# Performance work log

Measured on AMD Instinct MI355X. Metric: run time of the kernel, lower is better.

The kernel has to match this reference:

```python
import jax, jax.numpy as jnp
import numpy as np
from math import comb

B = 2048          # num_batch
NVAR = 11         # Bernstein coefficients per axis
NUM = 100         # trajectory time samples
NUM_OBS = 10
MAXITER = 50
T_FIN = 5.0
A_OBS = 0.4; B_OBS = 0.4
RHO_OBS = 1.0; RHO_INEQ = 1.0; RHO_TARGET = 1.0; RHO_PROJ = 1.0
V_MIN = 0.1; V_MAX = 2.0; A_MAX = 2.0


def _bernstein(n, t):
    return np.stack([comb(n, k) * t**k * (1.0 - t)**(n - k) for k in range(n + 1)], axis=1)


def _basis_matrices():
    # Bernstein polynomial basis of degree NVAR-1 sampled at NUM points over [0, T_FIN]
    t = np.linspace(0.0, 1.0, NUM)
    n = NVAR - 1
    P = _bernstein(n, t)
    Bm1 = _bernstein(n - 1, t)
    Bm2 = _bernstein(n - 2, t)
    dP = np.zeros_like(P); ddP = np.zeros_like(P)
    for k in range(n + 1):
        d = np.zeros(NUM)
        if k > 0: d += Bm1[:, k - 1]
        if k < n: d -= Bm1[:, k]
        dP[:, k] = n * d / T_FIN
        dd = np.zeros(NUM)
        if k > 1: dd += Bm2[:, k - 2]
        if 0 < k < n: dd -= 2.0 * Bm2[:, k - 1]
        if k < n - 1: dd += Bm2[:, k]
        ddP[:, k] = n * (n - 1) * dd / T_FIN**2
    return (jnp.asarray(P, jnp.float32), jnp.asarray(dP, jnp.float32), jnp.asarray(ddP, jnp.float32))


def setup_inputs() -> dict:
    key = jax.random.key(0)
    ks = jax.random.split(key, 10)
    P, Pdot, Pddot = _basis_matrices()
    u = lambda k, s, lo, hi: jax.random.uniform(k, s, jnp.float32, lo, hi)
    init_state_ego = jnp.concatenate([u(ks[0], (B, 2), -1.0, 1.0), u(ks[1], (B, 2), 0.1, 1.0)], axis=1)
    term_states = jnp.concatenate([u(ks[2], (B, 2), 2.0, 6.0), u(ks[3], (B, 2), 0.1, 1.0)], axis=1)
    via_points = u(ks[4], (B, 4), 0.5, 4.0)
    closest_obs = u(ks[5], (B, 2 * NUM_OBS), -4.0, 4.0)
    target_init = jnp.concatenate([u(ks[6], (B, 2), 1.0, 5.0), u(ks[7], (B, 2), -0.5, 0.5)], axis=1)
    d_min_t = u(ks[8], (B, 1), 1.0, 1.5)
    d_max_t = d_min_t + u(ks[9], (B, 1), 0.5, 1.0)
    d_target_bounds = jnp.concatenate([d_min_t, d_max_t], axis=1)
    return {"P": P, "Pdot": Pdot, "Pddot": Pddot, "init_state_ego": init_state_ego,
            "term_states": term_states, "via_points": via_points, "closest_obs": closest_obs,
            "target_init": target_init, "d_target_bounds": d_target_bounds}


def reference(P, Pdot, Pddot, init_state_ego, term_states, via_points, closest_obs, target_init, d_target_bounds):
    dt = P.dtype
    tot_time = jnp.linspace(0.0, T_FIN, NUM, dtype=dt)
    A_via = jnp.stack([P[49], P[74]])
    A_eq_init = jnp.vstack([P[0], Pdot[0], P[-1], Pdot[-1], A_via])   # [6, NVAR]
    A_eq = jnp.vstack([P[0], Pdot[0], P[-1], Pdot[-1]])               # [4, NVAR]
    A_obs_mat = jnp.tile(P, (NUM_OBS, 1))                             # [NUM_OBS*NUM, NVAR]
    A_vel, A_acc, A_target = Pdot, Pddot, P

    def kkt_inv(cost, A):
        m = A.shape[0]
        M = jnp.vstack([jnp.hstack([cost, A.T]), jnp.hstack([A, jnp.zeros((m, m), dt)])])
        return jnp.linalg.inv(M)

    inv_init = kkt_inv(Pddot.T @ Pddot, A_eq_init)
    cost_opt = (RHO_OBS * A_obs_mat.T @ A_obs_mat + RHO_INEQ * A_acc.T @ A_acc
                + RHO_INEQ * A_vel.T @ A_vel + RHO_TARGET * A_target.T @ A_target
                + RHO_PROJ * jnp.eye(NVAR, dtype=dt))
    inv_opt = kkt_inv(cost_opt, A_eq)

    zeros1 = jnp.zeros((B, 1), dt)
    vx0, vy0 = init_state_ego[:, 2:3], init_state_ego[:, 3:4]
    x_term, y_term = term_states[:, 0:1], term_states[:, 1:2]
    vx_term, vy_term = term_states[:, 2:3], term_states[:, 3:4]

    # warm-start QP (equality-constrained, zero linear cost): qp_layer_init
    b_eq_x_init = jnp.hstack([zeros1, vx0, x_term, vx_term, via_points[:, 0:2]])
    b_eq_y_init = jnp.hstack([zeros1, vy0, y_term, vy_term, via_points[:, 2:4]])
    zlin = jnp.zeros((B, NVAR), dt)
    c_x_bar = (jnp.hstack([zlin, b_eq_x_init]) @ inv_init.T)[:, :NVAR]
    c_y_bar = (jnp.hstack([zlin, b_eq_y_init]) @ inv_init.T)[:, :NVAR]

    b_eq_x = jnp.hstack([zeros1, vx0, x_term, vx_term])
    b_eq_y = jnp.hstack([zeros1, vy0, y_term, vy_term])

    # constant-velocity target trajectory, [B, NUM]
    x_target = target_init[:, 0:1] + target_init[:, 2:3] * tot_time[None, :]
    y_target = target_init[:, 1:2] + target_init[:, 3:4] * tot_time[None, :]

    # static obstacles tiled over time (obs-major, time fastest), [B, NUM_OBS*NUM]
    x_obs_traj = jnp.repeat(closest_obs[:, :NUM_OBS], NUM, axis=1)
    y_obs_traj = jnp.repeat(closest_obs[:, NUM_OBS:2 * NUM_OBS], NUM, axis=1)
    d_min_t, d_max_t = d_target_bounds[:, 0:1], d_target_bounds[:, 1:2]

    def step(carry, _):
        primal, lx, ly = carry
        cx, cy = primal[:, :NVAR], primal[:, NVAR:]
        x, xdot, xddot = cx @ P.T, cx @ Pdot.T, cx @ Pddot.T
        y, ydot, yddot = cy @ P.T, cy @ Pdot.T, cy @ Pddot.T
        # obstacle avoidance polar reformulation (compute_alph_d)
        wc = jnp.tile(x, (1, NUM_OBS)) - x_obs_traj
        ws = jnp.tile(y, (1, NUM_OBS)) - y_obs_traj
        a_o = jnp.arctan2(ws * A_OBS, wc * B_OBS)
        ca, sa = jnp.cos(a_o), jnp.sin(a_o)
        c1 = RHO_OBS * (A_OBS**2 * ca**2 + B_OBS**2 * sa**2)
        c2 = RHO_OBS * (A_OBS * wc * ca + B_OBS * ws * sa)
        d_obs = jnp.maximum(jnp.ones_like(c2), c2 / c1)
        # velocity bound (rho_ineq cancels in c2/c1)
        a_v = jnp.arctan2(ydot, xdot); cv, sv = jnp.cos(a_v), jnp.sin(a_v)
        d_v = jnp.clip(xdot * cv + ydot * sv, V_MIN, V_MAX)
        # acceleration bound
        a_a = jnp.arctan2(yddot, xddot); cA, sA = jnp.cos(a_a), jnp.sin(a_a)
        d_a = jnp.clip(xddot * cA + yddot * sA, 0.0, A_MAX)
        # target distance band
        wct, wst = x - x_target, y - y_target
        bt = jnp.arctan2(wst, wct); cb, sb = jnp.cos(bt), jnp.sin(bt)
        d_t = jnp.clip(wct * cb + wst * sb, d_min_t, d_max_t)
        # residuals -> dual (lambda) update
        res_xo = wc - A_OBS * d_obs * ca; res_yo = ws - B_OBS * d_obs * sa
        res_vx = xdot - d_v * cv;         res_vy = ydot - d_v * sv
        res_ax = xddot - d_a * cA;        res_ay = yddot - d_a * sA
        res_tx = wct - d_t * cb;          res_ty = wst - d_t * sb
        lx = lx - RHO_OBS * res_xo @ A_obs_mat - RHO_INEQ * res_ax @ A_acc - RHO_INEQ * res_vx @ A_vel - RHO_TARGET * res_tx @ A_target
        ly = ly - RHO_OBS * res_yo @ A_obs_mat - RHO_INEQ * res_ay @ A_acc - RHO_INEQ * res_vy @ A_vel - RHO_TARGET * res_ty @ A_target
        # linear cost and closed-form KKT solve (A_projection = I)
        b_ox = x_obs_traj + A_OBS * d_obs * ca; b_oy = y_obs_traj + B_OBS * d_obs * sa
        b_tx = x_target + d_t * cb;             b_ty = y_target + d_t * sb
        lin_x = (-lx - RHO_OBS * b_ox @ A_obs_mat - RHO_INEQ * (d_a * cA) @ A_acc
                 - RHO_INEQ * (d_v * cv) @ A_vel - RHO_TARGET * b_tx @ A_target - RHO_PROJ * c_x_bar)
        lin_y = (-ly - RHO_OBS * b_oy @ A_obs_mat - RHO_INEQ * (d_a * sA) @ A_acc
                 - RHO_INEQ * (d_v * sv) @ A_vel - RHO_TARGET * b_ty @ A_target - RHO_PROJ * c_y_bar)
        new_cx = (jnp.hstack([-lin_x, b_eq_x]) @ inv_opt.T)[:, :NVAR]
        new_cy = (jnp.hstack([-lin_y, b_eq_y]) @ inv_opt.T)[:, :NVAR]
        return (jnp.hstack([new_cx, new_cy]), lx, ly), None

    init = (jnp.hstack([c_x_bar, c_y_bar]), jnp.zeros((B, NVAR), dt), jnp.zeros((B, NVAR), dt))
    (primal, lx, ly), _ = jax.lax.scan(jax.checkpoint(step), init, None, length=MAXITER)
    return primal
```

## Files before the change

kernel.cpp:

```cpp
#include <hip/hip_runtime.h>
#include <math.h>

#define NVARS 11
#define NUMT  100
#define NOBS  10
#define MAXIT 50

#define E_OFF    0
#define F_OFF    66
#define G4_OFF   187
#define GP_OFF   231
#define GPD_OFF  352
#define GPDD_OFF 473
#define WS_FLOATS 594

__device__ void gj_inv(double (*aug)[34], int N, double* fac, int* piv, int tid, int nthr)
{
    for (int k = 0; k < N; ++k) {
        if (tid == 0) {
            int p = k; double best = fabs(aug[k][k]);
            for (int r = k + 1; r < N; ++r) { double v = fabs(aug[r][k]); if (v > best) { best = v; p = r; } }
            *piv = p;
        }
        __syncthreads();
        int p = *piv;
        if (p != k) {
            for (int c = tid; c < 2 * N; c += nthr) { double t = aug[k][c]; aug[k][c] = aug[p][c]; aug[p][c] = t; }
        }
        __syncthreads();
        double pv = aug[k][k];
        __syncthreads();
        for (int c = tid; c < 2 * N; c += nthr) aug[k][c] /= pv;
        __syncthreads();
        if (tid < N) fac[tid] = aug[tid][k];
        __syncthreads();
        for (int idx = tid; idx < N * 2 * N; idx += nthr) {
            int r = idx / (2 * N), c = idx % (2 * N);
            if (r != k) aug[r][c] -= fac[r] * aug[k][c];
        }
        __syncthreads();
    }
}

__global__ __launch_bounds__(128) void setup_kernel(const float* __restrict__ P,
                                                    const float* __restrict__ Pd,
                                                    const float* __restrict__ Pdd,
                                                    float* __restrict__ ws)
{
    __shared__ double G[3][NVARS][NVARS];
    __shared__ double aug[17][34];
    __shared__ double fac[17];
    __shared__ int piv;
    const int tid = threadIdx.x, nthr = 128;

    for (int idx = tid; idx < 3 * 121; idx += nthr) {
        int q = idx / 121, rem = idx % 121, r = rem / 11, c = rem % 11;
        const float* B = (q == 0) ? P : (q == 1) ? Pd : Pdd;
        double s = 0.0;
        for (int t = 0; t < NUMT; ++t) s += (double)B[t * 11 + r] * (double)B[t * 11 + c];
        G[q][r][c] = s;
    }
    __syncthreads();
    for (int idx = tid; idx < 3 * 121; idx += nthr) ws[GP_OFF + idx] = (float)((&G[0][0][0])[idx]);

    for (int idx = tid; idx < 17 * 34; idx += nthr) aug[idx / 34][idx % 34] = 0.0;
    __syncthreads();
    for (int idx = tid; idx < 121; idx += nthr) aug[idx / 11][idx % 11] = G[2][idx / 11][idx % 11];
    if (tid < 66) {
        int r = tid / 11, j = tid % 11;
        const float* src = (r == 0) ? P : (r == 1) ? Pd : (r == 2) ? (P + 99 * 11) : (r == 3) ? (Pd + 99 * 11)
                           : (r == 4) ? (P + 49 * 11) : (P + 74 * 11);
        double v = (double)src[j];
        aug[j][11 + r] = v;
        aug[11 + r][j] = v;
    }
    if (tid < 17) aug[tid][17 + tid] = 1.0;
    __syncthreads();
    gj_inv(aug, 17, fac, &piv, tid, nthr);
    if (tid < 66) { int j = tid / 6, k = tid % 6; ws[E_OFF + tid] = (float)aug[j][17 + 11 + k]; }
    __syncthreads();

    for (int idx = tid; idx < 17 * 34; idx += nthr) aug[idx / 34][idx % 34] = 0.0;
    __syncthreads();
    for (int idx = tid; idx < 121; idx += nthr) {
        int r = idx / 11, c = idx % 11;
        aug[r][c] = 11.0 * G[0][r][c] + G[1][r][c] + G[2][r][c] + ((r == c) ? 1.0 : 0.0);
    }
    if (tid < 44) {
        int r = tid / 11, j = tid % 11;
        const float* src = (r == 0) ? P : (r == 1) ? Pd : (r == 2) ? (P + 99 * 11) : (Pd + 99 * 11);
        double v = (double)src[j];
        aug[j][11 + r] = v;
        aug[11 + r][j] = v;
    }
    if (tid < 15) aug[tid][15 + tid] = 1.0;
    __syncthreads();
    gj_inv(aug, 15, fac, &piv, tid, nthr);
    if (tid < 121) { int j = tid / 11, k = tid % 11; ws[F_OFF + tid] = (float)aug[j][15 + k]; }
    if (tid < 44)  { int j = tid / 4,  k = tid % 4;  ws[G4_OFF + tid] = (float)aug[j][15 + 11 + k]; }
}

__device__ __forceinline__ float sbcast(float v) {
    return __int_as_float(__builtin_amdgcn_readfirstlane(__float_as_int(v)));
}

__global__ __launch_bounds__(256, 4) void solve_kernel(
    const float* __restrict__ P, const float* __restrict__ Pd, const float* __restrict__ Pdd,
    const float* __restrict__ ise, const float* __restrict__ term, const float* __restrict__ via,
    const float* __restrict__ obs, const float* __restrict__ tgt, const float* __restrict__ dtb,
    const float* __restrict__ ws, float* __restrict__ out, int Btot)
{
    __shared__ __align__(16) float sBc[NVARS][304];
    __shared__ __align__(16) float wbc[2][2][304];
    __shared__ float cst[WS_FLOATS];
    __shared__ float Dred[2][6][12];
    __shared__ float mlin[2][2][12];
    __shared__ float scoef[2][2][12];
    __shared__ float beqs[2][2][4];
    __shared__ float sobs[2][2][NOBS];
    __shared__ float stgt[2][6];

    const int tid = threadIdx.x;
    const int l = tid & 127;
    const int e = tid >> 7;
    int b = blockIdx.x * 2 + e;
    const bool real = (b < Btot);
    if (!real) b = Btot - 1;

    for (int idx = tid; idx < NVARS * 304; idx += 256) {
        int j = idx / 304, r = idx % 304;
        float v = 0.f;
        if (r < 300) {
            int q = r / 100, t = r % 100;
            const float* Bq = (q == 0) ? P : (q == 1) ? Pd : Pdd;
            v = Bq[t * 11 + j];
        }
        sBc[j][r] = v;
    }
    for (int idx = tid; idx < WS_FLOATS; idx += 256) cst[idx] = ws[idx];
    if (l < 20) sobs[e][l / 10][l % 10] = obs[b * 20 + l];
    if (l == 0) {
        beqs[e][0][0] = 0.f; beqs[e][0][1] = ise[b*4+2]; beqs[e][0][2] = term[b*4+0]; beqs[e][0][3] = term[b*4+2];
        beqs[e][1][0] = 0.f; beqs[e][1][1] = ise[b*4+3]; beqs[e][1][2] = term[b*4+1]; beqs[e][1][3] = term[b*4+3];
        stgt[e][0] = tgt[b*4+0]; stgt[e][1] = tgt[b*4+2];
        stgt[e][2] = tgt[b*4+1]; stgt[e][3] = tgt[b*4+3];
        stgt[e][4] = dtb[b*2+0]; stgt[e][5] = dtb[b*2+1];
    }
    __syncthreads();

    const int ca = l / 11, cj = l % 11;
    float lm = 0.f, cb = 0.f;
    if (l < 22) {
        float bi0 = 0.f, bi1 = beqs[e][ca][1], bi2 = beqs[e][ca][2], bi3 = beqs[e][ca][3];
        float bi4 = via[b*4 + 2*ca + 0], bi5 = via[b*4 + 2*ca + 1];
        const float* E = &cst[E_OFF + cj * 6];
        float s = E[0]*bi0 + E[1]*bi1 + E[2]*bi2 + E[3]*bi3 + E[4]*bi4 + E[5]*bi5;
        cb = s; scoef[e][ca][cj] = s;
    }

    float rP[NVARS], rPd[NVARS], rPdd[NVARS];
    {
        const int t = (l < NUMT) ? l : 0;
        #pragma unroll
        for (int k = 0; k < NVARS; ++k) {
            rP[k]   = sBc[k][t];
            rPd[k]  = sBc[k][t + 100];
            rPdd[k] = sBc[k][t + 200];
        }
    }
    float obx[NOBS], oby[NOBS];
    #pragma unroll
    for (int o = 0; o < NOBS; ++o) {
        obx[o] = sbcast(sobs[e][0][o]);
        oby[o] = sbcast(sobs[e][1][o]);
    }
    const float tg0 = sbcast(stgt[e][0]), tg1 = sbcast(stgt[e][1]);
    const float tg2 = sbcast(stgt[e][2]), tg3 = sbcast(stgt[e][3]);
    const float tg4 = sbcast(stgt[e][4]), tg5 = sbcast(stgt[e][5]);

    float* pwA = &wbc[e][0][l];
    const int wi = l % 6, bjj = l / 6;
    const float4* pbB = (const float4*)(&sBc[0][0] + bjj * 304 + (wi % 3) * 100);
    const float4* pwB = (const float4*)(&wbc[e][wi / 3][(wi % 3) * 100]);
    __syncthreads();

    for (int it = 0; it < MAXIT; ++it) {
        if (l < NUMT) {
            float x=0,y=0,xd=0,yd=0,xdd=0,ydd=0;
            #pragma unroll
            for (int k = 0; k < NVARS; ++k) {
                float cxk = scoef[e][0][k], cyk = scoef[e][1][k];
                x += cxk*rP[k];   y += cyk*rP[k];
                xd += cxk*rPd[k]; yd += cyk*rPd[k];
                xdd += cxk*rPdd[k]; ydd += cyk*rPdd[k];
            }
            float Sbx = 0.f, Sby = 0.f;
            #pragma unroll
            for (int o = 0; o < NOBS; ++o) {
                float dx = x - obx[o], dy = y - oby[o];
                float r2 = dx*dx + dy*dy;
                float f  = fmaxf(1.0f, 0.4f * rsqrtf(fmaxf(r2, 1e-30f)));
                Sbx += fmaf(dx, f, obx[o]);
                Sby += fmaf(dy, f, oby[o]);
            }
            float rv = sqrtf(xd*xd + yd*yd);
            float fv = fminf(fmaxf(rv, 0.1f), 2.0f) / fmaxf(rv, 1e-30f);
            float ra = sqrtf(xdd*xdd + ydd*ydd);
            float fa = fminf(ra, 2.0f) / fmaxf(ra, 1e-30f);
            float tt = (float)l * (5.0f / 99.0f);
            float xt = tg0 + tg1*tt, yt = tg2 + tg3*tt;
            float wct = x - xt, wst = y - yt;
            float rt = sqrtf(wct*wct + wst*wst);
            float ftg = fminf(fmaxf(rt, tg4), tg5) / fmaxf(rt, 1e-30f);
            pwA[0]   = Sbx + xt + wct*ftg;
            pwA[100] = xd * fv;
            pwA[200] = xdd * fa;
            pwA[304] = Sby + yt + wst*ftg;
            pwA[404] = yd * fv;
            pwA[504] = ydd * fa;
        }
        __syncthreads();

        if (l < 66) {
            float s = 0.f;
            #pragma unroll
            for (int i = 0; i < 25; ++i) {
                float4 a = pbB[i], w = pwB[i];
                s += w.x * a.x; s += w.y * a.y; s += w.z * a.z; s += w.w * a.w;
            }
            Dred[e][wi][bjj] = s;
        }
        __syncthreads();

        if (l < 22) {
            float d4=0.f, d5=0.f, d6=0.f;
            #pragma unroll
            for (int k = 0; k < 11; ++k) {
                float ck = scoef[e][ca][k];
                d4 += ck * cst[GP_OFF   + k*11 + cj];
                d5 += ck * cst[GPD_OFF  + k*11 + cj];
                d6 += ck * cst[GPDD_OFF + k*11 + cj];
            }
            int i0 = 3*ca;
            float D0 = Dred[e][i0][cj], D1 = Dred[e][i0+1][cj], D2 = Dred[e][i0+2][cj];
            lm -= (11.f*d4 - D0) + (d5 - D1) + (d6 - D2);
            mlin[e][ca][cj] = lm + D0 + D1 + D2 + cb;
        }

        if (l < 22) {
            float s = 0.f;
            #pragma unroll
            for (int k = 0; k < 11; ++k) s += cst[F_OFF + cj*11 + k] * mlin[e][ca][k];
            #pragma unroll
            for (int k = 0; k < 4; ++k)  s += cst[G4_OFF + cj*4 + k] * beqs[e][ca][k];
            scoef[e][ca][cj] = s;
        }
        __syncthreads();
    }

    if (real && l < 22) out[b * 22 + l] = scoef[e][ca][cj];
}

extern "C" void kernel_launch(void* const* d_in, const int* in_sizes, int n_in,
                              void* d_out, int out_size, void* d_ws, size_t ws_size,
                              hipStream_t stream)
{
    const float* P    = (const float*)d_in[0];
    const float* Pd   = (const float*)d_in[1];
    const float* Pdd  = (const float*)d_in[2];
    const float* ise  = (const float*)d_in[3];
    const float* term = (const float*)d_in[4];
    const float* via  = (const float*)d_in[5];
    const float* obs  = (const float*)d_in[6];
    const float* tgt  = (const float*)d_in[7];
    const float* dtb  = (const float*)d_in[8];
    float* ws  = (float*)d_ws;
    float* out = (float*)d_out;

    const int B = in_sizes[3] / 4;
    const int nblk = (B + 1) / 2;

    hipLaunchKernelGGL(setup_kernel, dim3(1), dim3(128), 0, stream, P, Pd, Pdd, ws);
    hipLaunchKernelGGL(solve_kernel, dim3(nblk), dim3(256), 0, stream,
                       P, Pd, Pdd, ise, term, via, obs, tgt, dtb, ws, out, B);
}
```

Baseline: 263.6 us.

## Use one batch element per block and overlap Gram products with trajectory eval

Each 256-thread block now handles a single batch element instead of two, doubling the grid, and launch bounds now request 8 blocks per CU. The coefficient-times-Gram products (d4/d5/d6) move to threads 128-149, so they run during the trajectory/projection phase instead of serially after the reduction. The intent is to shorten the per-iteration critical path and raise parallelism. In exchange, each block still loads the full basis tables into shared memory for only one element, and threads 100-127 and 150-255 sit idle, wasting lanes.

```diff
diff --git a/kernel.cpp b/kernel.cpp
--- a/kernel.cpp
+++ b/kernel.cpp
@@ -104,28 +104,25 @@
     return __int_as_float(__builtin_amdgcn_readfirstlane(__float_as_int(v)));
 }
 
-__global__ __launch_bounds__(256, 4) void solve_kernel(
+__global__ __launch_bounds__(256, 8) void solve_kernel(
     const float* __restrict__ P, const float* __restrict__ Pd, const float* __restrict__ Pdd,
     const float* __restrict__ ise, const float* __restrict__ term, const float* __restrict__ via,
     const float* __restrict__ obs, const float* __restrict__ tgt, const float* __restrict__ dtb,
-    const float* __restrict__ ws, float* __restrict__ out, int Btot)
+    const float* __restrict__ ws, float* __restrict__ out)
 {
     __shared__ __align__(16) float sBc[NVARS][304];
-    __shared__ __align__(16) float wbc[2][2][304];
+    __shared__ __align__(16) float wbc[2][304];
     __shared__ float cst[WS_FLOATS];
-    __shared__ float Dred[2][6][12];
-    __shared__ float mlin[2][2][12];
-    __shared__ float scoef[2][2][12];
-    __shared__ float beqs[2][2][4];
-    __shared__ float sobs[2][2][NOBS];
-    __shared__ float stgt[2][6];
+    __shared__ float sd456[3][24];
+    __shared__ float Dred[6][12];
+    __shared__ float mlin[2][12];
+    __shared__ float scoef[2][12];
+    __shared__ float beqs[2][4];
+    __shared__ float sobs[2][NOBS];
+    __shared__ float stgt[6];
 
     const int tid = threadIdx.x;
-    const int l = tid & 127;
-    const int e = tid >> 7;
-    int b = blockIdx.x * 2 + e;
-    const bool real = (b < Btot);
-    if (!real) b = Btot - 1;
+    const int b = blockIdx.x;
 
     for (int idx = tid; idx < NVARS * 304; idx += 256) {
         int j = idx / 304, r = idx % 304;
@@ -138,29 +135,29 @@
         sBc[j][r] = v;
     }
     for (int idx = tid; idx < WS_FLOATS; idx += 256) cst[idx] = ws[idx];
-    if (l < 20) sobs[e][l / 10][l % 10] = obs[b * 20 + l];
-    if (l == 0) {
-        beqs[e][0][0] = 0.f; beqs[e][0][1] = ise[b*4+2]; beqs[e][0][2] = term[b*4+0]; beqs[e][0][3] = term[b*4+2];
-        beqs[e][1][0] = 0.f; beqs[e][1][1] = ise[b*4+3]; beqs[e][1][2] = term[b*4+1]; beqs[e][1][3] = term[b*4+3];
-        stgt[e][0] = tgt[b*4+0]; stgt[e][1] = tgt[b*4+2];
-        stgt[e][2] = tgt[b*4+1]; stgt[e][3] = tgt[b*4+3];
-        stgt[e][4] = dtb[b*2+0]; stgt[e][5] = dtb[b*2+1];
-    }
-    __syncthreads();
-
-    const int ca = l / 11, cj = l % 11;
+    if (tid < 20) sobs[tid / 10][tid % 10] = obs[b * 20 + tid];
+    if (tid == 0) {
+        beqs[0][0] = 0.f; beqs[0][1] = ise[b*4+2]; beqs[0][2] = term[b*4+0]; beqs[0][3] = term[b*4+2];
+        beqs[1][0] = 0.f; beqs[1][1] = ise[b*4+3]; beqs[1][2] = term[b*4+1]; beqs[1][3] = term[b*4+3];
+        stgt[0] = tgt[b*4+0]; stgt[1] = tgt[b*4+2];
+        stgt[2] = tgt[b*4+1]; stgt[3] = tgt[b*4+3];
+        stgt[4] = dtb[b*2+0]; stgt[5] = dtb[b*2+1];
+    }
+    __syncthreads();
+
+    const int ca = tid / 11, cj = tid % 11;
     float lm = 0.f, cb = 0.f;
-    if (l < 22) {
-        float bi0 = 0.f, bi1 = beqs[e][ca][1], bi2 = beqs[e][ca][2], bi3 = beqs[e][ca][3];
+    if (tid < 22) {
+        float bi0 = 0.f, bi1 = beqs[ca][1], bi2 = beqs[ca][2], bi3 = beqs[ca][3];
         float bi4 = via[b*4 + 2*ca + 0], bi5 = via[b*4 + 2*ca + 1];
         const float* E = &cst[E_OFF + cj * 6];
         float s = E[0]*bi0 + E[1]*bi1 + E[2]*bi2 + E[3]*bi3 + E[4]*bi4 + E[5]*bi5;
-        cb = s; scoef[e][ca][cj] = s;
+        cb = s; scoef[ca][cj] = s;
     }
 
     float rP[NVARS], rPd[NVARS], rPdd[NVARS];
     {
-        const int t = (l < NUMT) ? l : 0;
+        const int t = (tid < NUMT) ? tid : 0;
         #pragma unroll
         for (int k = 0; k < NVARS; ++k) {
             rP[k]   = sBc[k][t];
@@ -171,25 +168,26 @@
     float obx[NOBS], oby[NOBS];
     #pragma unroll
     for (int o = 0; o < NOBS; ++o) {
-        obx[o] = sbcast(sobs[e][0][o]);
-        oby[o] = sbcast(sobs[e][1][o]);
-    }
-    const float tg0 = sbcast(stgt[e][0]), tg1 = sbcast(stgt[e][1]);
-    const float tg2 = sbcast(stgt[e][2]), tg3 = sbcast(stgt[e][3]);
-    const float tg4 = sbcast(stgt[e][4]), tg5 = sbcast(stgt[e][5]);
-
-    float* pwA = &wbc[e][0][l];
-    const int wi = l % 6, bjj = l / 6;
+        obx[o] = sbcast(sobs[0][o]);
+        oby[o] = sbcast(sobs[1][o]);
+    }
+    const float tg0 = sbcast(stgt[0]), tg1 = sbcast(stgt[1]);
+    const float tg2 = sbcast(stgt[2]), tg3 = sbcast(stgt[3]);
+    const float tg4 = sbcast(stgt[4]), tg5 = sbcast(stgt[5]);
+
+    float* pwA = &wbc[0][tid];
+    const int wi = tid % 6, bjj = tid / 6;
     const float4* pbB = (const float4*)(&sBc[0][0] + bjj * 304 + (wi % 3) * 100);
-    const float4* pwB = (const float4*)(&wbc[e][wi / 3][(wi % 3) * 100]);
+    const float4* pwB = (const float4*)(&wbc[wi / 3][(wi % 3) * 100]);
+    const int l2 = tid - 128;
     __syncthreads();
 
     for (int it = 0; it < MAXIT; ++it) {
-        if (l < NUMT) {
+        if (tid < NUMT) {
             float x=0,y=0,xd=0,yd=0,xdd=0,ydd=0;
             #pragma unroll
             for (int k = 0; k < NVARS; ++k) {
-                float cxk = scoef[e][0][k], cyk = scoef[e][1][k];
+                float cxk = scoef[0][k], cyk = scoef[1][k];
                 x += cxk*rP[k];   y += cyk*rP[k];
                 xd += cxk*rPd[k]; yd += cyk*rPd[k];
                 xdd += cxk*rPdd[k]; ydd += cyk*rPdd[k];
@@ -207,7 +205,7 @@
             float fv = fminf(fmaxf(rv, 0.1f), 2.0f) / fmaxf(rv, 1e-30f);
             float ra = sqrtf(xdd*xdd + ydd*ydd);
             float fa = fminf(ra, 2.0f) / fmaxf(ra, 1e-30f);
-            float tt = (float)l * (5.0f / 99.0f);
+            float tt = (float)tid * (5.0f / 99.0f);
             float xt = tg0 + tg1*tt, yt = tg2 + tg3*tt;
             float wct = x - xt, wst = y - yt;
             float rt = sqrtf(wct*wct + wst*wst);
@@ -219,46 +217,51 @@
             pwA[404] = yd * fv;
             pwA[504] = ydd * fa;
         }
-        __syncthreads();
-
-        if (l < 66) {
+        if (l2 >= 0 && l2 < 22) {
+            const int ga = l2 / 11, gj = l2 % 11;
+            float d4=0.f, d5=0.f, d6=0.f;
+            #pragma unroll
+            for (int k = 0; k < 11; ++k) {
+                float ck = scoef[ga][k];
+                d4 += ck * cst[GP_OFF   + k*11 + gj];
+                d5 += ck * cst[GPD_OFF  + k*11 + gj];
+                d6 += ck * cst[GPDD_OFF + k*11 + gj];
+            }
+            sd456[0][l2] = d4; sd456[1][l2] = d5; sd456[2][l2] = d6;
+        }
+        __syncthreads();
+
+        if (tid < 66) {
             float s = 0.f;
             #pragma unroll
             for (int i = 0; i < 25; ++i) {
                 float4 a = pbB[i], w = pwB[i];
                 s += w.x * a.x; s += w.y * a.y; s += w.z * a.z; s += w.w * a.w;
             }
-            Dred[e][wi][bjj] = s;
-        }
-        __syncthreads();
-
-        if (l < 22) {
-            float d4=0.f, d5=0.f, d6=0.f;
-            #pragma unroll
-            for (int k = 0; k < 11; ++k) {
-                float ck = scoef[e][ca][k];
-                d4 += ck * cst[GP_OFF   + k*11 + cj];
-                d5 += ck * cst[GPD_OFF  + k*11 + cj];
-                d6 += ck * cst[GPDD_OFF + k*11 + cj];
-            }
+            Dred[wi][bjj] = s;
+        }
+        __syncthreads();
+
+        if (tid < 22) {
+            float d4 = sd456[0][tid], d5 = sd456[1][tid], d6 = sd456[2][tid];
             int i0 = 3*ca;
-            float D0 = Dred[e][i0][cj], D1 = Dred[e][i0+1][cj], D2 = Dred[e][i0+2][cj];
+            float D0 = Dred[i0][cj], D1 = Dred[i0+1][cj], D2 = Dred[i0+2][cj];
             lm -= (11.f*d4 - D0) + (d5 - D1) + (d6 - D2);
-            mlin[e][ca][cj] = lm + D0 + D1 + D2 + cb;
-        }
-
-        if (l < 22) {
+            mlin[ca][cj] = lm + D0 + D1 + D2 + cb;
+        }
+
+        if (tid < 22) {
             float s = 0.f;
             #pragma unroll
-            for (int k = 0; k < 11; ++k) s += cst[F_OFF + cj*11 + k] * mlin[e][ca][k];
-            #pragma unroll
-            for (int k = 0; k < 4; ++k)  s += cst[G4_OFF + cj*4 + k] * beqs[e][ca][k];
-            scoef[e][ca][cj] = s;
-        }
-        __syncthreads();
-    }
-
-    if (real && l < 22) out[b * 22 + l] = scoef[e][ca][cj];
+            for (int k = 0; k < 11; ++k) s += cst[F_OFF + cj*11 + k] * mlin[ca][k];
+            #pragma unroll
+            for (int k = 0; k < 4; ++k)  s += cst[G4_OFF + cj*4 + k] * beqs[ca][k];
+            scoef[ca][cj] = s;
+        }
+        __syncthreads();
+    }
+
+    if (tid < 22) out[b * 22 + tid] = scoef[ca][cj];
 }
 
 extern "C" void kernel_launch(void* const* d_in, const int* in_sizes, int n_in,
@@ -278,9 +281,8 @@
     float* out = (float*)d_out;
 
     const int B = in_sizes[3] / 4;
-    const int nblk = (B + 1) / 2;
 
     hipLaunchKernelGGL(setup_kernel, dim3(1), dim3(128), 0, stream, P, Pd, Pdd, ws);
-    hipLaunchKernelGGL(solve_kernel, dim3(nblk), dim3(256), 0, stream,
-                       P, Pd, Pdd, ise, term, via, obs, tgt, dtb, ws, out, B);
-}
+    hipLaunchKernelGGL(solve_kernel, dim3(B), dim3(256), 0, stream,
+                       P, Pd, Pdd, ise, term, via, obs, tgt, dtb, ws, out);
+}
```

After: 267.8 us. About the same (+1.6%).
